# Kernel optimization log

Measured on AMD Instinct MI355X. Metric: run time of the kernel, lower is better.

The kernel has to match this reference:

```python
import jax, jax.numpy as jnp
import numpy as np

K = 4  # kernel_size

def setup_inputs() -> dict:
    key = jax.random.key(0)
    k1, k2, k3 = jax.random.split(key, 3)
    B, T, C = 4, 4096, 2048
    x = jax.random.normal(k1, (B, T, C), dtype=jnp.float32)
    # depthwise Conv1d weight (C, 1, K) flattened to (C, K); PyTorch default init scale
    bound = 1.0 / np.sqrt(K)
    weight = jax.random.uniform(k2, (C, K), dtype=jnp.float32, minval=-bound, maxval=bound)
    bias = jax.random.uniform(k3, (C,), dtype=jnp.float32, minval=-bound, maxval=bound)
    return {"x": x, "weight": weight, "bias": bias}

def reference(x, weight, bias):
    # Causal depthwise conv on (B,T,C) directly (no transpose needed in jax):
    # y[b,t,c] = sum_k weight[c,k] * x[b, t-(K-1)+k, c] + bias[c]; out = x + y
    B, T, C = x.shape
    xp = jnp.pad(x, ((0, 0), (K - 1, 0), (0, 0)))  # left-pad time axis
    y = bias[None, None, :]
    for k in range(K):  # small fixed kernel taps
        y = y + xp[:, k:k + T, :] * weight[None, None, :, k]
    return x + y
```

## Files before the change

kernel.cpp:

```cpp
#include <hip/hip_runtime.h>

#define B_DIM 4
#define T_DIM 4096
#define C_DIM 2048
#define KK 4
#define TT 16
#define C4 (C_DIM / 4)

typedef float v4f __attribute__((ext_vector_type(4)));

__global__ __launch_bounds__(256) void canonconv_kernel(
    const float* __restrict__ x,
    const float* __restrict__ w,
    const float* __restrict__ bias,
    float* __restrict__ out)
{
    const int idx   = blockIdx.x * blockDim.x + threadIdx.x;
    const int c4    = idx % C4;
    const int tmp   = idx / C4;
    const int ttile = tmp % (T_DIM / TT);
    const int b     = tmp / (T_DIM / TT);
    const int t0    = ttile * TT;
    const int c     = c4 * 4;

    const v4f* wv = (const v4f*)(w + (size_t)c * KK);
    const v4f a0 = wv[0];
    const v4f a1 = wv[1];
    const v4f a2 = wv[2];
    const v4f a3 = wv[3];
    const v4f bv = *(const v4f*)(bias + c);

    const float* xb = x   + ((size_t)b * T_DIM) * C_DIM + c;
    float*       ob = out + ((size_t)b * T_DIM) * C_DIM + c;

    v4f xm3, xm2, xm1;
    const bool interior = (t0 != 0);
    if (interior) {
        xm3 = *(const v4f*)(xb + (size_t)(t0 - 3) * C_DIM);
        xm2 = *(const v4f*)(xb + (size_t)(t0 - 2) * C_DIM);
        xm1 = *(const v4f*)(xb + (size_t)(t0 - 1) * C_DIM);
    }

    v4f buf[TT];
    #pragma unroll
    for (int j = 0; j < TT; ++j) {
        buf[j] = *(const v4f*)(xb + (size_t)(t0 + j) * C_DIM);
    }

    if (!interior) {
        xm3 = (v4f)0.0f;
        xm2 = (v4f)0.0f;
        xm1 = (v4f)0.0f;
    }

    v4f tap0, tap1, tap2, tap3;
    tap0.x = a0.x; tap0.y = a1.x; tap0.z = a2.x; tap0.w = a3.x;
    tap1.x = a0.y; tap1.y = a1.y; tap1.z = a2.y; tap1.w = a3.y;
    tap2.x = a0.z; tap2.y = a1.z; tap2.z = a2.z; tap2.w = a3.z;
    tap3.x = 1.0f + a0.w; tap3.y = 1.0f + a1.w; tap3.z = 1.0f + a2.w; tap3.w = 1.0f + a3.w;

    #pragma unroll
    for (int j = 0; j < TT; ++j) {
        const v4f xc = buf[j];
        v4f r;
        r.x = fmaf(xc.x, tap3.x, fmaf(xm1.x, tap2.x, fmaf(xm2.x, tap1.x, fmaf(xm3.x, tap0.x, bv.x))));
        r.y = fmaf(xc.y, tap3.y, fmaf(xm1.y, tap2.y, fmaf(xm2.y, tap1.y, fmaf(xm3.y, tap0.y, bv.y))));
        r.z = fmaf(xc.z, tap3.z, fmaf(xm1.z, tap2.z, fmaf(xm2.z, tap1.z, fmaf(xm3.z, tap0.z, bv.z))));
        r.w = fmaf(xc.w, tap3.w, fmaf(xm1.w, tap2.w, fmaf(xm2.w, tap1.w, fmaf(xm3.w, tap0.w, bv.w))));
        *(v4f*)(ob + (size_t)(t0 + j) * C_DIM) = r;
        xm3 = xm2;
        xm2 = xm1;
        xm1 = xc;
    }
}

extern "C" void kernel_launch(void* const* d_in, const int* in_sizes, int n_in,
                              void* d_out, int out_size, void* d_ws, size_t ws_size,
                              hipStream_t stream) {
    const float* x    = (const float*)d_in[0];
    const float* w    = (const float*)d_in[1];
    const float* bias = (const float*)d_in[2];
    float* out = (float*)d_out;

    const int total_threads = B_DIM * (T_DIM / TT) * C4;
    const int block = 256;
    const int grid  = total_threads / block;
    canonconv_kernel<<<grid, block, 0, stream>>>(x, w, bias, out);
}
```

Baseline: 236.8 us.

## Map one vector per thread and swizzle blocks across XCDs for L2 reuse

Each thread now computes a single float4 output instead of a 16-step time tile, reading its own row plus the three previous rows straight from global memory. Those neighbour reads are expected to hit in cache rather than DRAM. Blocks are remapped so that each XCD gets a contiguous range of rows, which keeps the time-shifted neighbour loads in the same XCD's L2. The aim is more memory parallelism and better occupancy than the register-heavy tiled version. The cost is four times as many load instructions, more threads and blocks, and a dependence on L2 hit rates.

```diff
diff --git a/kernel.cpp b/kernel.cpp
--- a/kernel.cpp
+++ b/kernel.cpp
@@ -4,8 +4,13 @@
 #define T_DIM 4096
 #define C_DIM 2048
 #define KK 4
-#define TT 16
 #define C4 (C_DIM / 4)
+#define ROWS (B_DIM * T_DIM)
+#define NV4 (ROWS * C4)
+#define BLOCK 256
+#define NBLK (NV4 / BLOCK)
+#define NXCD 8
+#define BPX (NBLK / NXCD)
 
 typedef float v4f __attribute__((ext_vector_type(4)));
 
@@ -15,13 +20,21 @@
     const float* __restrict__ bias,
     float* __restrict__ out)
 {
-    const int idx   = blockIdx.x * blockDim.x + threadIdx.x;
-    const int c4    = idx % C4;
-    const int tmp   = idx / C4;
-    const int ttile = tmp % (T_DIM / TT);
-    const int b     = tmp / (T_DIM / TT);
-    const int t0    = ttile * TT;
-    const int c     = c4 * 4;
+    const int bid = blockIdx.x;
+    const int swz = (bid & (NXCD - 1)) * BPX + (bid >> 3);
+    const int p   = swz * BLOCK + threadIdx.x;
+    const int c4  = p & (C4 - 1);
+    const int row = p >> 9;
+    const int t   = row & (T_DIM - 1);
+    const int c   = c4 * 4;
+
+    const v4f* xv = (const v4f*)x;
+
+    const v4f xc = xv[p];
+    v4f xm1 = (v4f)0.0f, xm2 = (v4f)0.0f, xm3 = (v4f)0.0f;
+    if (t >= 1) xm1 = xv[p - C4];
+    if (t >= 2) xm2 = xv[p - 2 * C4];
+    if (t >= 3) xm3 = xv[p - 3 * C4];
 
     const v4f* wv = (const v4f*)(w + (size_t)c * KK);
     const v4f a0 = wv[0];
@@ -30,48 +43,13 @@
     const v4f a3 = wv[3];
     const v4f bv = *(const v4f*)(bias + c);
 
-    const float* xb = x   + ((size_t)b * T_DIM) * C_DIM + c;
-    float*       ob = out + ((size_t)b * T_DIM) * C_DIM + c;
+    v4f r;
+    r.x = fmaf(xc.x, 1.0f + a0.w, fmaf(xm1.x, a0.z, fmaf(xm2.x, a0.y, fmaf(xm3.x, a0.x, bv.x))));
+    r.y = fmaf(xc.y, 1.0f + a1.w, fmaf(xm1.y, a1.z, fmaf(xm2.y, a1.y, fmaf(xm3.y, a1.x, bv.y))));
+    r.z = fmaf(xc.z, 1.0f + a2.w, fmaf(xm1.z, a2.z, fmaf(xm2.z, a2.y, fmaf(xm3.z, a2.x, bv.z))));
+    r.w = fmaf(xc.w, 1.0f + a3.w, fmaf(xm1.w, a3.z, fmaf(xm2.w, a3.y, fmaf(xm3.w, a3.x, bv.w))));
 
-    v4f xm3, xm2, xm1;
-    const bool interior = (t0 != 0);
-    if (interior) {
-        xm3 = *(const v4f*)(xb + (size_t)(t0 - 3) * C_DIM);
-        xm2 = *(const v4f*)(xb + (size_t)(t0 - 2) * C_DIM);
-        xm1 = *(const v4f*)(xb + (size_t)(t0 - 1) * C_DIM);
-    }
-
-    v4f buf[TT];
-    #pragma unroll
-    for (int j = 0; j < TT; ++j) {
-        buf[j] = *(const v4f*)(xb + (size_t)(t0 + j) * C_DIM);
-    }
-
-    if (!interior) {
-        xm3 = (v4f)0.0f;
-        xm2 = (v4f)0.0f;
-        xm1 = (v4f)0.0f;
-    }
-
-    v4f tap0, tap1, tap2, tap3;
-    tap0.x = a0.x; tap0.y = a1.x; tap0.z = a2.x; tap0.w = a3.x;
-    tap1.x = a0.y; tap1.y = a1.y; tap1.z = a2.y; tap1.w = a3.y;
-    tap2.x = a0.z; tap2.y = a1.z; tap2.z = a2.z; tap2.w = a3.z;
-    tap3.x = 1.0f + a0.w; tap3.y = 1.0f + a1.w; tap3.z = 1.0f + a2.w; tap3.w = 1.0f + a3.w;
-
-    #pragma unroll
-    for (int j = 0; j < TT; ++j) {
-        const v4f xc = buf[j];
-        v4f r;
-        r.x = fmaf(xc.x, tap3.x, fmaf(xm1.x, tap2.x, fmaf(xm2.x, tap1.x, fmaf(xm3.x, tap0.x, bv.x))));
-        r.y = fmaf(xc.y, tap3.y, fmaf(xm1.y, tap2.y, fmaf(xm2.y, tap1.y, fmaf(xm3.y, tap0.y, bv.y))));
-        r.z = fmaf(xc.z, tap3.z, fmaf(xm1.z, tap2.z, fmaf(xm2.z, tap1.z, fmaf(xm3.z, tap0.z, bv.z))));
-        r.w = fmaf(xc.w, tap3.w, fmaf(xm1.w, tap2.w, fmaf(xm2.w, tap1.w, fmaf(xm3.w, tap0.w, bv.w))));
-        *(v4f*)(ob + (size_t)(t0 + j) * C_DIM) = r;
-        xm3 = xm2;
-        xm2 = xm1;
-        xm1 = xc;
-    }
+    ((v4f*)out)[p] = r;
 }
 
 extern "C" void kernel_launch(void* const* d_in, const int* in_sizes, int n_in,
@@ -82,8 +60,5 @@
     const float* bias = (const float*)d_in[2];
     float* out = (float*)d_out;
 
-    const int total_threads = B_DIM * (T_DIM / TT) * C4;
-    const int block = 256;
-    const int grid  = total_threads / block;
-    canonconv_kernel<<<grid, block, 0, stream>>>(x, w, bias, out);
+    canonconv_kernel<<<NBLK, BLOCK, 0, stream>>>(x, w, bias, out);
 }
```

New measurement: 287.9 us. 21.6% more time.
